# Optimization experiments

Measured on AMD Instinct MI355X. Metric: run time of the kernel, lower is better.

## Reference

```python
import jax, jax.numpy as jnp
import numpy as np

B, T, D, H = 2, 1024, 1024, 16
K = D            # key_dim = hidden * expand_k (1.0)
V = 2 * D        # value_dim = hidden * expand_v (2.0)
DK, DV = K // H, V // H
I = 2816         # SwiGLU intermediate
CONV = 4
EPS = 1e-6


def rmsnorm(x, w, eps=EPS):
    return x * jax.lax.rsqrt(jnp.mean(x * x, -1, keepdims=True) + eps) * w


def l2norm(x, eps=EPS):
    return x * jax.lax.rsqrt(jnp.sum(x * x, -1, keepdims=True) + eps)


def short_conv(x, w):
    # depthwise causal conv1d (kernel CONV, no bias) + silu; x [B,T,C], w [C,CONV]
    kern = w.T[:, None, :]  # [CONV, 1, C]
    y = jax.lax.conv_general_dilated(
        x, kern, (1,), [(CONV - 1, 0)],
        dimension_numbers=('NWC', 'WIO', 'NWC'),
        feature_group_count=x.shape[-1])
    return jax.nn.silu(y)


def setup_inputs() -> dict:
    key = jax.random.key(0)
    ks = jax.random.split(key, 20)
    p = lambda i, shape, s=0.02: jax.random.normal(ks[i], shape, jnp.float32) * s
    return dict(
        x=jax.random.normal(ks[0], (B, T, D), jnp.float32),
        norm1_w=jnp.ones((D,), jnp.float32),
        wq=p(1, (D, K)), wk=p(2, (D, K)), wv=p(3, (D, V)),
        conv_q=p(4, (K, CONV), 0.3), conv_k=p(5, (K, CONV), 0.3), conv_v=p(6, (V, CONV), 0.3),
        wb=p(7, (D, H)), wa=p(8, (D, H)),
        A_log=jnp.log(jax.random.uniform(ks[9], (H,), jnp.float32, 1.0, 16.0)),
        dt_bias=jnp.log(jnp.expm1(jax.random.uniform(ks[10], (H,), jnp.float32, 0.001, 0.1))),
        wg=p(11, (D, V)),
        o_norm_w=jnp.ones((DV,), jnp.float32),
        wo=p(12, (V, D)),
        norm2_w=jnp.ones((D,), jnp.float32),
        w1=p(13, (D, I)), w2=p(14, (I, D)), w3=p(15, (D, I)),
    )


def reference(x, norm1_w, wq, wk, wv, conv_q, conv_k, conv_v, wb, wa,
              A_log, dt_bias, wg, o_norm_w, wo, norm2_w, w1, w2, w3):
    h = rmsnorm(x, norm1_w)
    # projections + short causal conv (silu)
    q = short_conv(h @ wq, conv_q).reshape(B, T, H, DK)
    k = short_conv(h @ wk, conv_k).reshape(B, T, H, DK)
    v = short_conv(h @ wv, conv_v).reshape(B, T, H, DV)
    q = l2norm(q) * (DK ** -0.5)
    k = l2norm(k)
    beta = jax.nn.sigmoid(h @ wb)                              # [B,T,H]
    # mamba-style decay gate: g = -exp(A_log) * softplus(a + dt_bias)
    g = -jnp.exp(A_log) * jax.nn.softplus(h @ wa + dt_bias)   # [B,T,H]

    # gated delta rule: S_t = exp(g_t)*S_{t-1}; u_t = beta_t*(v_t - k_t^T S_t);
    # S_t += k_t u_t^T; o_t = q_t^T S_t
    def step(S, inp):
        qt, kt, vt, gt, bt = inp                               # [B,H,*]
        S = S * jnp.exp(gt)[..., None, None]
        u = (vt - jnp.einsum('bhk,bhkv->bhv', kt, S)) * bt[..., None]
        S = S + kt[..., None] * u[:, :, None, :]
        ot = jnp.einsum('bhk,bhkv->bhv', qt, S)
        return S, ot

    S0 = jnp.zeros((B, H, DK, DV), x.dtype)
    seq = (q.transpose(1, 0, 2, 3), k.transpose(1, 0, 2, 3),
           v.transpose(1, 0, 2, 3), g.transpose(1, 0, 2), beta.transpose(1, 0, 2))
    _, o = jax.lax.scan(step, S0, seq)
    o = o.transpose(1, 0, 2, 3)                                # [B,T,H,DV]

    # output gate: per-head RMSNorm * swish(gate), then out-projection
    gate = (h @ wg).reshape(B, T, H, DV)
    o = rmsnorm(o, o_norm_w) * gate * jax.nn.sigmoid(gate)
    x = x + o.reshape(B, T, V) @ wo

    # SwiGLU MLP with residual
    h2 = rmsnorm(x, norm2_w)
    return x + (jax.nn.silu(h2 @ w1) * (h2 @ w3)) @ w2
```

## Files before the change

kernel.cpp:

```cpp
#include <hip/hip_runtime.h>
#include <stdint.h>

typedef unsigned short u16;
typedef float f32x4 __attribute__((ext_vector_type(4)));
typedef __bf16 bf16x8 __attribute__((ext_vector_type(8)));
typedef unsigned short u16x8 __attribute__((ext_vector_type(8)));

#define N1P 6400

__device__ __forceinline__ u16 f2bf(float f) {
    union { float f; uint32_t u; } v; v.f = f;
    uint32_t u = v.u;
    return (u16)((u + 0x7FFFu + ((u >> 16) & 1u)) >> 16);
}
__device__ __forceinline__ float bf2f(u16 h) {
    union { uint32_t u; float f; } v; v.u = ((uint32_t)h) << 16; return v.f;
}
__device__ __forceinline__ float sigm(float x) { return 1.f / (1.f + __expf(-x)); }

__device__ __forceinline__ void async16(const u16* g, u16* l) {
    __builtin_amdgcn_global_load_lds((const __attribute__((address_space(1))) void*)g,
                                     (__attribute__((address_space(3))) void*)l, 16, 0, 0);
}

__device__ __forceinline__ int swz64(int row, int col) {
    return row * 128 + ((((col >> 3) ^ (row & 7)) << 3) + (col & 7)) * 2;
}
__device__ __forceinline__ bf16x8 frag64(const u16* m, int rowbase, int lane, int kk) {
    const int row = rowbase + (lane & 15);
    const int unit = (lane >> 4) + (kk << 2);
    return *(const bf16x8*)((const char*)m + row * 128 + ((unit ^ (row & 7)) << 4));
}

struct TJob { const float* src; u16* dst; int rows, cols, rowOff, rowStride, nOut, blkBase, gx, mode; };
struct TJobs { TJob j[10]; };

__global__ __launch_bounds__(256) void k_transpose_all(TJobs jobs, int njobs) {
    __shared__ float tile[32][33];
    const int bid = blockIdx.x;
    int ji = 0;
#pragma unroll
    for (int i = 1; i < 10; ++i)
        if (i < njobs && bid >= jobs.j[i].blkBase) ji = i;
    const TJob J = jobs.j[ji];
    const int bx = bid - J.blkBase;
    const int n0 = (bx % J.gx) * 32, k0 = (bx / J.gx) * 32;
    const int tx = threadIdx.x, ty = threadIdx.y;
#pragma unroll
    for (int j = 0; j < 32; j += 8) {
        int r = k0 + ty + j, c = n0 + tx;
        tile[ty + j][tx] = (r < J.rows && c < J.cols) ? J.src[(size_t)r * J.cols + c] : 0.f;
    }
    __syncthreads();
#pragma unroll
    for (int j = 0; j < 32; j += 8) {
        int n = n0 + ty + j, k = k0 + tx;
        if (n < J.nOut) {
            int drow = (J.mode == 0) ? (J.rowOff + n * J.rowStride)
                                     : (J.rowOff + ((n >> 4) << 5) + (n & 15));
            J.dst[(size_t)drow * J.rows + k] = f2bf(tile[tx][ty + j]);
        }
    }
}

__global__ __launch_bounds__(256) void k_rmsnorm(const float* __restrict__ x, const float* __restrict__ w,
                                                 u16* __restrict__ out) {
    const int row = blockIdx.x, tid = threadIdx.x, lane = tid & 63, wave = tid >> 6;
    const float4 v = ((const float4*)(x + (size_t)row * 1024))[tid];
    float ss = v.x * v.x + v.y * v.y + v.z * v.z + v.w * v.w;
#pragma unroll
    for (int o = 1; o < 64; o <<= 1) ss += __shfl_xor(ss, o);
    __shared__ float sred[4];
    if (lane == 0) sred[wave] = ss;
    __syncthreads();
    const float tot = sred[0] + sred[1] + sred[2] + sred[3];
    const float rn = rsqrtf(tot * (1.f / 1024.f) + 1e-6f);
    const float4 wv = ((const float4*)w)[tid];
    uint2 pk;
    pk.x = (uint32_t)f2bf(v.x * rn * wv.x) | ((uint32_t)f2bf(v.y * rn * wv.y) << 16);
    pk.y = (uint32_t)f2bf(v.z * rn * wv.z) | ((uint32_t)f2bf(v.w * rn * wv.w) << 16);
    *(uint2*)&out[(size_t)row * 1024 + tid * 4] = pk;
}

template <int EPI>
__global__ __launch_bounds__(512, 2) void k_gemm256(const u16* __restrict__ A, const u16* __restrict__ Bt,
                                                    u16* __restrict__ Cout, int N, int Kd) {
    __shared__ __align__(16) u16 L[65536];
    const int q8 = (int)gridDim.x >> 3;
    const int bid = blockIdx.x;
    const int wg = (bid & 7) * q8 + (bid >> 3);
    const int bm = wg & 7, bn = wg >> 3;
    const int tid = threadIdx.x, lane = tid & 63, wave = tid >> 6;
    const int wm = wave >> 2, wn = wave & 3;

    const int scol = ((tid & 7) ^ ((tid >> 3) & 7)) * 8;
    const u16* gA = A + (size_t)(bm * 256 + (tid >> 3)) * Kd + scol;
    const u16* gB = Bt + (size_t)(bn * 256 + (tid >> 3)) * Kd + scol;
    u16* dstT = L + tid * 8;

    const int NT = Kd >> 6;
    const int NI = NT >> 1;

    auto issue = [&](const u16* g, int mtx, int kt, int h) {
        u16* d = dstT + (kt & 1) * 32768 + mtx * 16384 + h * 8192;
        const u16* s = g + (size_t)(h * 128) * Kd + kt * 64;
        async16(s, d);
        async16(s + (size_t)64 * Kd, d + 4096);
    };

    issue(gB, 1, 0, 0); issue(gB, 1, 0, 1);
    issue(gA, 0, 0, 0); issue(gA, 0, 0, 1);
    issue(gB, 1, 1, 0); issue(gB, 1, 1, 1);
    asm volatile("s_waitcnt vmcnt(4)" ::: "memory");
    __builtin_amdgcn_s_barrier();

    f32x4 acc[8][4] = {};
    bf16x8 bq[4][2];

    for (int i = 0; i < NI; ++i) {
        const int kt0 = 2 * i;
#pragma unroll
        for (int p = 0; p < 8; ++p) {
            const int half = p >> 2;
            const int q = p & 3;
            const u16* Ab = L + half * 32768;
            const u16* Bb = L + half * 32768 + 16384;
            if (q == 0) {
#pragma unroll
                for (int ni = 0; ni < 4; ++ni)
#pragma unroll
                    for (int kk = 0; kk < 2; ++kk)
                        bq[ni][kk] = frag64(Bb, wn * 64 + ni * 16, lane, kk);
            }
            bf16x8 af[2][2];
#pragma unroll
            for (int j = 0; j < 2; ++j)
#pragma unroll
                for (int kk = 0; kk < 2; ++kk)
                    af[j][kk] = frag64(Ab, wm * 128 + (2 * q + j) * 16, lane, kk);
            if (p == 0) { if (kt0 + 1 < NT) issue(gA, 0, kt0 + 1, 0); }
            if (p == 1) { if (kt0 + 1 < NT) issue(gA, 0, kt0 + 1, 1);
                          if (kt0 + 2 < NT) issue(gB, 1, kt0 + 2, 0); }
            if (p == 2) { if (kt0 + 2 < NT) issue(gB, 1, kt0 + 2, 1); }
            if (p == 4) { if (kt0 + 2 < NT) issue(gA, 0, kt0 + 2, 0); }
            if (p == 5) { if (kt0 + 2 < NT) issue(gA, 0, kt0 + 2, 1);
                          if (kt0 + 3 < NT) issue(gB, 1, kt0 + 3, 0); }
            if (p == 6) { if (kt0 + 3 < NT) issue(gB, 1, kt0 + 3, 1); }
            if (p == 3) { if (i + 1 < NI) { asm volatile("s_waitcnt vmcnt(4)" ::: "memory"); }
                          else            { asm volatile("s_waitcnt vmcnt(0)" ::: "memory"); } }
            if (p == 7) { if (i + 1 < NI) { asm volatile("s_waitcnt vmcnt(4)" ::: "memory"); } }
            __builtin_amdgcn_s_barrier();
            __builtin_amdgcn_s_setprio(1);
#pragma unroll
            for (int j = 0; j < 2; ++j)
#pragma unroll
                for (int ni = 0; ni < 4; ++ni)
#pragma unroll
                    for (int kk = 0; kk < 2; ++kk)
                        acc[2 * q + j][ni] = __builtin_amdgcn_mfma_f32_16x16x32_bf16(
                            af[j][kk], bq[ni][kk], acc[2 * q + j][ni], 0, 0, 0);
            __builtin_amdgcn_s_setprio(0);
            __builtin_amdgcn_s_barrier();
        }
    }

    const int rsub = (lane >> 4) * 4, csub = lane & 15;
    if constexpr (EPI == 2) {
        u16* ct = L;
#pragma unroll
        for (int r = 0; r < 2; ++r) {
            if (wm == r) {
#pragma unroll
                for (int mi = 0; mi < 8; ++mi)
#pragma unroll
                    for (int ni = 0; ni < 4; ++ni)
#pragma unroll
                        for (int rr = 0; rr < 4; ++rr)
                            ct[(mi * 16 + rsub + rr) * 264 + wn * 64 + ni * 16 + csub] =
                                f2bf(acc[mi][ni][rr]);
            }
            __syncthreads();
#pragma unroll
            for (int k = 0; k < 8; ++k) {
                const int f = (tid + k * 512) * 8;
                const int r2 = f >> 8, c = f & 255;
                *(u16x8*)&Cout[(size_t)(bm * 256 + r * 128 + r2) * N + bn * 256 + c] =
                    *(const u16x8*)&ct[r2 * 264 + c];
            }
            __syncthreads();
        }
    } else {
        u16* ct = L;
#pragma unroll
        for (int mi = 0; mi < 8; ++mi)
#pragma unroll
            for (int g = 0; g < 2; ++g)
#pragma unroll
                for (int rr = 0; rr < 4; ++rr) {
                    const float u1 = acc[mi][2 * g][rr];
                    const float u3 = acc[mi][2 * g + 1][rr];
                    ct[(wm * 128 + mi * 16 + rsub + rr) * 132 + wn * 32 + g * 16 + csub] =
                        f2bf(u1 * sigm(u1) * u3);
                }
        __syncthreads();
#pragma unroll
        for (int k = 0; k < 8; ++k) {
            const int f = (tid + k * 512) * 8;
            const int r2 = f >> 7, c = f & 127;
            *(u16x8*)&Cout[(size_t)(bm * 256 + r2) * N + bn * 128 + c] =
                *(const u16x8*)&ct[r2 * 132 + c];
        }
    }
}

template <int TILE, int EPI>
__global__ __launch_bounds__(512) void k_gemm(const u16* __restrict__ A, const u16* __restrict__ Bt,
                                              void* __restrict__ Cout, const float* __restrict__ Res,
                                              int N, int Kd) {
    __shared__ __align__(16) char smem[TILE * 512];
    u16* Asb = (u16*)smem;
    u16* Bsb = (u16*)(smem + TILE * 256);
    constexpr int MB = 2048 / TILE;
    const int q = (int)gridDim.x >> 3;
    const int bid = blockIdx.x;
    const int wg = (bid & 7) * q + (bid >> 3);
    const int bm = wg & (MB - 1), bn = wg / MB;
    const int tid = threadIdx.x, lane = tid & 63, wave = tid >> 6;
    const int wm = wave >> 2, wn = wave & 3;
    constexpr int RS = TILE / 2, CS = TILE / 4;
    constexpr int FRM = RS / 16, FRN = CS / 16;
    constexpr int IS = TILE / 64;

    const int srow = wave * 8 + (lane >> 3);
    const int scol = ((lane & 7) ^ (lane >> 3)) * 8;
    const u16* gA = A + (size_t)(bm * TILE + srow) * Kd + scol;
    const u16* gB = Bt + (size_t)(bn * TILE + srow) * Kd + scol;

    f32x4 acc[FRM][FRN] = {};
    const int NT = Kd >> 6;

#pragma unroll
    for (int j = 0; j < IS; ++j) {
        async16(gA + (size_t)j * 64 * Kd, Asb + j * 4096 + wave * 512);
        async16(gB + (size_t)j * 64 * Kd, Bsb + j * 4096 + wave * 512);
    }
    asm volatile("s_waitcnt vmcnt(0)" ::: "memory");
    __syncthreads();

    int buf = 0;
    for (int t = 0; t < NT; ++t) {
        if (t + 1 < NT) {
            const int k0 = (t + 1) << 6;
            const int bo = (buf ^ 1) * TILE * 64;
#pragma unroll
            for (int j = 0; j < IS; ++j) {
                async16(gA + (size_t)j * 64 * Kd + k0, Asb + bo + j * 4096 + wave * 512);
                async16(gB + (size_t)j * 64 * Kd + k0, Bsb + bo + j * 4096 + wave * 512);
            }
        }
        const u16* Ab = Asb + buf * TILE * 64;
        const u16* Bb = Bsb + buf * TILE * 64;
#pragma unroll
        for (int kk = 0; kk < 2; ++kk) {
            bf16x8 af[FRM], bfr[FRN];
#pragma unroll
            for (int mi = 0; mi < FRM; ++mi) af[mi] = frag64(Ab, wm * RS + mi * 16, lane, kk);
#pragma unroll
            for (int ni = 0; ni < FRN; ++ni) bfr[ni] = frag64(Bb, wn * CS + ni * 16, lane, kk);
#pragma unroll
            for (int mi = 0; mi < FRM; ++mi)
#pragma unroll
                for (int ni = 0; ni < FRN; ++ni)
                    acc[mi][ni] = __builtin_amdgcn_mfma_f32_16x16x32_bf16(af[mi], bfr[ni], acc[mi][ni], 0, 0, 0);
        }
        asm volatile("s_waitcnt vmcnt(0)" ::: "memory");
        __syncthreads();
        buf ^= 1;
    }

    const int rsub = (lane >> 4) * 4;
    const int csub = lane & 15;
    float* ctile = (float*)smem;
#pragma unroll
    for (int mi = 0; mi < FRM; ++mi)
#pragma unroll
        for (int ni = 0; ni < FRN; ++ni)
#pragma unroll
            for (int r = 0; r < 4; ++r)
                ctile[(wm * 32 + mi * 16 + rsub + r) * 68 + wn * 16 + ni * 16 + csub] = acc[mi][ni][r];
    __syncthreads();
#pragma unroll
    for (int k = 0; k < 2; ++k) {
        const int f = (tid + k * 512) * 4;
        const int r = f >> 6, c = f & 63;
        float4 v = *(const float4*)&ctile[r * 68 + c];
        const float4 rv = *(const float4*)&Res[(size_t)(bm * 64 + r) * N + bn * 64 + c];
        v.x += rv.x; v.y += rv.y; v.z += rv.z; v.w += rv.w;
        *(float4*)&((float*)Cout)[(size_t)(bm * 64 + r) * N + bn * 64 + c] = v;
    }
}

__global__ __launch_bounds__(256) void k_conv(const u16* __restrict__ P, const float* __restrict__ cwq,
                                              const float* __restrict__ cwk, const float* __restrict__ cwv,
                                              const float* __restrict__ A_log, const float* __restrict__ dtb,
                                              u16* __restrict__ Qb, u16* __restrict__ Kb,
                                              u16* __restrict__ Vb, float* __restrict__ Gl,
                                              float* __restrict__ Bbuf) {
    const int bid = blockIdx.x;
    const int row = (bid & 7) * 256 + (bid >> 3);
    const int t = row & 1023;
    const int tid = threadIdx.x;
    const long prow = (long)row * N1P;
#pragma unroll
    for (int p = 0; p < 2; ++p) {
        const int g = p * 256 + tid;
        const int c = g * 8;
        u16x8 taps[4];
#pragma unroll
        for (int j = 0; j < 4; ++j) {
            const int tt = t - 3 + j;
            if (tt >= 0) taps[j] = *(const u16x8*)&P[prow + (long)(j - 3) * N1P + c];
            else         taps[j] = u16x8{};
        }
        const float* cw = (c < 1024) ? (cwq + c * 4)
                          : (c < 2048) ? (cwk + (c - 1024) * 4)
                                       : (cwv + (c - 2048) * 4);
        float y[8];
#pragma unroll
        for (int e = 0; e < 8; ++e) {
            const float4 w = ((const float4*)cw)[e];
            float v = bf2f(taps[0][e]) * w.x + bf2f(taps[1][e]) * w.y +
                      bf2f(taps[2][e]) * w.z + bf2f(taps[3][e]) * w.w;
            y[e] = v * sigm(v);
        }
        if (c < 2048) {
            float ss = 0.f;
#pragma unroll
            for (int e = 0; e < 8; ++e) ss += y[e] * y[e];
            ss += __shfl_xor(ss, 1); ss += __shfl_xor(ss, 2); ss += __shfl_xor(ss, 4);
            const float rn = rsqrtf(ss + 1e-6f);
            const float sc = (c < 1024) ? rn * 0.125f : rn;
            u16x8 o;
#pragma unroll
            for (int e = 0; e < 8; ++e) o[e] = f2bf(y[e] * sc);
            if (c < 1024) *(u16x8*)&Qb[(size_t)row * 1024 + c] = o;
            else          *(u16x8*)&Kb[(size_t)row * 1024 + (c - 1024)] = o;
        } else {
            u16x8 o;
#pragma unroll
            for (int e = 0; e < 8; ++e) o[e] = f2bf(y[e]);
            *(u16x8*)&Vb[(size_t)row * 2048 + (c - 2048)] = o;
        }
    }
    if (tid < 32) {
        const int h = tid & 15;
        const float val = bf2f(P[prow + 4096 + tid]);
        if (tid < 16) {
            Bbuf[(size_t)row * 16 + h] = sigm(val);
        } else {
            const float a = val + dtb[h];
            const float sp = (a > 15.f) ? a : log1pf(__expf(a));
            Gl[(size_t)row * 16 + h] = -__expf(A_log[h]) * sp;
        }
    }
}

__global__ __launch_bounds__(256) void k_scan1(
    const u16* __restrict__ Qb, const u16* __restrict__ Kb, const u16* __restrict__ Vb,
    const float* __restrict__ Gl, const float* __restrict__ Bb,
    u16* __restrict__ CHW, u16* __restrict__ CHM, u16* __restrict__ CHQc,
    u16* __restrict__ CHKcT, u16* __restrict__ CHU0T, float* __restrict__ CHcC) {
    __shared__ __align__(16) char sm[66048];
    u16* Ql   = (u16*)(sm);
    u16* Kl   = (u16*)(sm + 8192);
    u16* VTb  = (u16*)(sm + 16384);
    u16* KT1b = (u16*)(sm + 32768);
    u16* Mim  = (u16*)(sm + 40960);
    u16* MTim = (u16*)(sm + 49152);
    u16* Tb   = (u16*)(sm + 57344);
    float* Tl    = (float*)sm;
    float* gcs   = (float*)(sm + 65536);
    float* betal = (float*)(sm + 65792);

    const int blk = blockIdx.x;
    const int bb = blk >> 8, h = (blk >> 4) & 15, ch = blk & 15;
    const int bhc = blk;
    const int tid = threadIdx.x, lane = tid & 63, wave = tid >> 6;
    const long rowbase = (long)bb * 1024 + ch * 64;

    if (tid < 64) {
        gcs[tid] = Gl[(rowbase + tid) * 16 + h];
        betal[tid] = Bb[(rowbase + tid) * 16 + h];
    }
    for (int u = tid; u < 512; u += 256) {
        int r = u >> 3, c8 = u & 7;
        uint4 kv = *(const uint4*)&Kb[(rowbase + r) * 1024 + h * 64 + c8 * 8];
        uint4 qv = *(const uint4*)&Qb[(rowbase + r) * 1024 + h * 64 + c8 * 8];
        int b = r * 128 + ((c8 ^ (r & 7)) << 4);
        *(uint4*)((char*)Kl + b) = kv;
        *(uint4*)((char*)Ql + b) = qv;
    }
    __syncthreads();
    if (wave == 0) {
        float g = gcs[lane];
#pragma unroll
        for (int off = 1; off < 64; off <<= 1) {
            float n = __shfl_up(g, off, 64);
            if (lane >= off) g += n;
        }
        gcs[lane] = g;
    }
    for (int u = tid; u < 1024; u += 256) {
        int r = u >> 4, c8 = u & 15;
        u16x8 vv = *(const u16x8*)&Vb[(rowbase + r) * 2048 + h * 128 + c8 * 8];
        float bsc = betal[r];
#pragma unroll
        for (int j = 0; j < 8; ++j) {
            int dv = c8 * 8 + j;
            *(u16*)((char*)VTb + swz64(dv, r)) = f2bf(bf2f(vv[j]) * bsc);
        }
    }
    f32x4 aQK[4] = {}, aKK[4] = {};
#pragma unroll
    for (int nt = 0; nt < 4; ++nt)
#pragma unroll
        for (int kk = 0; kk < 2; ++kk) {
            bf16x8 bq = frag64(Kl, nt * 16, lane, kk);
            aQK[nt] = __builtin_amdgcn_mfma_f32_16x16x32_bf16(frag64(Ql, wave * 16, lane, kk), bq, aQK[nt], 0, 0, 0);
            aKK[nt] = __builtin_amdgcn_mfma_f32_16x16x32_bf16(frag64(Kl, wave * 16, lane, kk), bq, aKK[nt], 0, 0, 0);
        }
    __syncthreads();

    const float gcsC = gcs[63];
    float am[4][4];
#pragma unroll
    for (int nt = 0; nt < 4; ++nt)
#pragma unroll
        for (int reg = 0; reg < 4; ++reg) {
            int t = wave * 16 + ((lane >> 4) << 2) + reg;
            int i = nt * 16 + (lane & 15);
            float dec = __expf(gcs[t] - gcs[i]);
            float mv = (i <= t) ? dec * aQK[nt][reg] : 0.f;
            *(u16*)((char*)CHM + (size_t)bhc * 8192 + swz64(t, i)) = f2bf(mv);
            float a = (i < t) ? betal[t] * dec * aKK[nt][reg] : 0.f;
            am[nt][reg] = -a;
            u16 amb = f2bf(-a);
            *(u16*)((char*)Mim + swz64(t, i)) = amb;
            *(u16*)((char*)MTim + swz64(i, t)) = amb;
        }
    for (int e = tid; e < 4096; e += 256) {
        int r = e >> 6, c = e & 63;
        int ib = swz64(r, c);
        float qv = bf2f(*(const u16*)((const char*)Ql + ib)) * __expf(gcs[r]);
        *(u16*)((char*)CHQc + (size_t)bhc * 8192 + ib) = f2bf(qv);
        float kv = bf2f(*(const u16*)((const char*)Kl + ib));
        int ob = swz64(c, r);
        *(u16*)((char*)KT1b + ob) = f2bf(kv * betal[r] * __expf(gcs[r]));
        *(u16*)((char*)CHKcT + (size_t)bhc * 8192 + ob) = f2bf(kv * __expf(gcsC - gcs[r]));
    }
    if (tid == 0) CHcC[bhc] = __expf(gcsC);
    __syncthreads();

#pragma unroll
    for (int nt = 0; nt < 4; ++nt)
#pragma unroll
        for (int reg = 0; reg < 4; ++reg) {
            int t = wave * 16 + ((lane >> 4) << 2) + reg;
            int i = nt * 16 + (lane & 15);
            float tv = (t == i) ? 1.f : am[nt][reg];
            Tl[t * 64 + i] = tv;
            *(u16*)((char*)Tb + swz64(t, i)) = f2bf(tv);
        }
    __syncthreads();

    const int hi = wave * 16 + 15;
#pragma unroll
    for (int j = 1; j <= 5; ++j) {
        f32x4 aM[4] = {};
#pragma unroll
        for (int nt = 0; nt < 4; ++nt) {
            if (nt * 16 > hi - (1 << j)) continue;
#pragma unroll
            for (int kk = 0; kk < 2; ++kk) {
                if (kk * 32 > hi) break;
                aM[nt] = __builtin_amdgcn_mfma_f32_16x16x32_bf16(
                    frag64(Mim, wave * 16, lane, kk), frag64(MTim, nt * 16, lane, kk), aM[nt], 0, 0, 0);
            }
        }
        __syncthreads();
#pragma unroll
        for (int nt = 0; nt < 4; ++nt)
#pragma unroll
            for (int reg = 0; reg < 4; ++reg) {
                int t = wave * 16 + ((lane >> 4) << 2) + reg;
                int i = nt * 16 + (lane & 15);
                float mv = (t - i >= (1 << j)) ? aM[nt][reg] : 0.f;
                u16 mb = f2bf(mv);
                *(u16*)((char*)Mim + swz64(t, i)) = mb;
                *(u16*)((char*)MTim + swz64(i, t)) = mb;
            }
        __syncthreads();
        f32x4 aT[4];
#pragma unroll
        for (int nt = 0; nt < 4; ++nt)
#pragma unroll
            for (int reg = 0; reg < 4; ++reg) {
                int t = wave * 16 + ((lane >> 4) << 2) + reg;
                int i = nt * 16 + (lane & 15);
                aT[nt][reg] = Tl[t * 64 + i];
            }
#pragma unroll
        for (int nt = 0; nt < 4; ++nt) {
            if (nt * 16 > hi - (1 << j)) continue;
#pragma unroll
            for (int kk = 0; kk < 2; ++kk) {
                if (kk * 32 > hi) break;
                aT[nt] = __builtin_amdgcn_mfma_f32_16x16x32_bf16(
                    frag64(Tb, wave * 16, lane, kk), frag64(MTim, nt * 16, lane, kk), aT[nt], 0, 0, 0);
            }
        }
#pragma unroll
        for (int nt = 0; nt < 4; ++nt)
#pragma unroll
            for (int reg = 0; reg < 4; ++reg) {
                int t = wave * 16 + ((lane >> 4) << 2) + reg;
                int i = nt * 16 + (lane & 15);
                Tl[t * 64 + i] = aT[nt][reg];
                *(u16*)((char*)Tb + swz64(t, i)) = f2bf(aT[nt][reg]);
            }
    }
    __syncthreads();

    {
        f32x4 aW[4] = {};
#pragma unroll
        for (int nt = 0; nt < 4; ++nt)
#pragma unroll
            for (int kk = 0; kk < 2; ++kk) {
                if (kk * 32 > hi) break;
                aW[nt] = __builtin_amdgcn_mfma_f32_16x16x32_bf16(
                    frag64(Tb, wave * 16, lane, kk), frag64(KT1b, nt * 16, lane, kk), aW[nt], 0, 0, 0);
            }
#pragma unroll
        for (int nt = 0; nt < 4; ++nt)
#pragma unroll
            for (int reg = 0; reg < 4; ++reg) {
                int r = wave * 16 + ((lane >> 4) << 2) + reg;
                int c = nt * 16 + (lane & 15);
                *(u16*)((char*)CHW + (size_t)bhc * 8192 + swz64(r, c)) = f2bf(aW[nt][reg]);
            }
    }
#pragma unroll
    for (int rt = 0; rt < 2; ++rt) {
        f32x4 aU[4] = {};
        int rb = (wave * 2 + rt) * 16;
#pragma unroll
        for (int nt = 0; nt < 4; ++nt)
#pragma unroll
            for (int kk = 0; kk < 2; ++kk) {
                if (kk * 32 > nt * 16 + 15) continue;
                aU[nt] = __builtin_amdgcn_mfma_f32_16x16x32_bf16(
                    frag64(VTb, rb, lane, kk), frag64(Tb, nt * 16, lane, kk), aU[nt], 0, 0, 0);
            }
#pragma unroll
        for (int nt = 0; nt < 4; ++nt)
#pragma unroll
            for (int reg = 0; reg < 4; ++reg) {
                int dv = rb + ((lane >> 4) << 2) + reg;
                int c = nt * 16 + (lane & 15);
                *(u16*)((char*)CHU0T + (size_t)bhc * 16384 + swz64(dv, c)) = f2bf(aU[nt][reg]);
            }
    }
}

__global__ __launch_bounds__(256) void k_scan2(
    const u16* __restrict__ CHW, const u16* __restrict__ CHM, const u16* __restrict__ CHQc,
    const u16* __restrict__ CHKcT, const u16* __restrict__ CHU0T, const float* __restrict__ CHcC,
    float* __restrict__ O) {
    __shared__ __align__(16) u16 stg[2][5 * 4096];
    __shared__ __align__(16) u16 STb[4096], uTl[4096];
    __shared__ float ST[64 * 66];
    const int blk = blockIdx.x;
    const int bb = blk >> 5, h = (blk >> 1) & 15, dvh = blk & 1;
    const int bh = bb * 16 + h;
    const int tid = threadIdx.x, lane = tid & 63, wave = tid >> 6;

    for (int e = tid; e < 64 * 66; e += 256) ST[e] = 0.f;
    for (int e = tid; e < 4096; e += 256) STb[e] = 0;

    auto stage = [&](int buf, int ch) {
        const size_t base = (size_t)(bh * 16 + ch);
        const u16* srcs[5] = { CHW + base * 4096, CHM + base * 4096, CHQc + base * 4096,
                               CHKcT + base * 4096, CHU0T + base * 8192 + dvh * 4096 };
#pragma unroll
        for (int s = 0; s < 5; ++s)
#pragma unroll
            for (int r = 0; r < 2; ++r) {
                int ub = r * 256 + wave * 64;
                async16(srcs[s] + (size_t)(ub + lane) * 8, &stg[buf][s * 4096 + ub * 8]);
            }
    };
    stage(0, 0);
    for (int ch = 0; ch < 16; ++ch) {
        const int cur = ch & 1;
        asm volatile("s_waitcnt vmcnt(0)" ::: "memory");
        __syncthreads();
        if (ch < 15) stage(cur ^ 1, ch + 1);
        const u16* sW = &stg[cur][0];
        const u16* sM = &stg[cur][4096];
        const u16* sQc = &stg[cur][8192];
        const u16* sKcT = &stg[cur][12288];
        const u16* sU0 = &stg[cur][16384];
        {
            f32x4 acc[4] = {};
#pragma unroll
            for (int nt = 0; nt < 4; ++nt)
#pragma unroll
                for (int kk = 0; kk < 2; ++kk)
                    acc[nt] = __builtin_amdgcn_mfma_f32_16x16x32_bf16(
                        frag64(STb, wave * 16, lane, kk), frag64(sW, nt * 16, lane, kk), acc[nt], 0, 0, 0);
#pragma unroll
            for (int nt = 0; nt < 4; ++nt)
#pragma unroll
                for (int reg = 0; reg < 4; ++reg) {
                    int dv = wave * 16 + ((lane >> 4) << 2) + reg;
                    int c = nt * 16 + (lane & 15);
                    int b = swz64(dv, c);
                    float u0 = bf2f(*(const u16*)((const char*)sU0 + b));
                    *(u16*)((char*)uTl + b) = f2bf(u0 - acc[nt][reg]);
                }
        }
        __syncthreads();
        f32x4 accO[4] = {}, accS[4] = {};
#pragma unroll
        for (int nt = 0; nt < 4; ++nt)
#pragma unroll
            for (int kk = 0; kk < 2; ++kk) {
                accO[nt] = __builtin_amdgcn_mfma_f32_16x16x32_bf16(
                    frag64(sM, wave * 16, lane, kk), frag64(uTl, nt * 16, lane, kk), accO[nt], 0, 0, 0);
                accO[nt] = __builtin_amdgcn_mfma_f32_16x16x32_bf16(
                    frag64(sQc, wave * 16, lane, kk), frag64(STb, nt * 16, lane, kk), accO[nt], 0, 0, 0);
                accS[nt] = __builtin_amdgcn_mfma_f32_16x16x32_bf16(
                    frag64(uTl, wave * 16, lane, kk), frag64(sKcT, nt * 16, lane, kk), accS[nt], 0, 0, 0);
            }
        __syncthreads();
        const float cC = CHcC[bh * 16 + ch];
#pragma unroll
        for (int nt = 0; nt < 4; ++nt)
#pragma unroll
            for (int reg = 0; reg < 4; ++reg) {
                int rr = wave * 16 + ((lane >> 4) << 2) + reg;
                int cc = nt * 16 + (lane & 15);
                O[((size_t)(bb * 1024 + ch * 64 + rr)) * 2048 + h * 128 + dvh * 64 + cc] = accO[nt][reg];
                float ns = cC * ST[rr * 66 + cc] + accS[nt][reg];
                ST[rr * 66 + cc] = ns;
                *(u16*)((char*)STb + swz64(rr, cc)) = f2bf(ns);
            }
    }
}

__global__ __launch_bounds__(256) void k_gate(const float* __restrict__ O, const u16* __restrict__ P,
                                              const float* __restrict__ onw, u16* __restrict__ OG) {
    const int row = blockIdx.x;
    const int tid = threadIdx.x, lane = tid & 63, wave = tid >> 6;
#pragma unroll
    for (int p = 0; p < 4; ++p) {
        const int h = p * 4 + wave;
        const int dv = lane * 2;
        const float2 o2 = *(const float2*)&O[(size_t)row * 2048 + h * 128 + dv];
        float ss = o2.x * o2.x + o2.y * o2.y;
#pragma unroll
        for (int o = 1; o < 64; o <<= 1) ss += __shfl_xor(ss, o);
        const float rn = rsqrtf(ss * (1.f / 128.f) + 1e-6f);
        const float g0 = bf2f(P[(size_t)row * N1P + 4128 + h * 128 + dv]);
        const float g1 = bf2f(P[(size_t)row * N1P + 4128 + h * 128 + dv + 1]);
        const float r0 = o2.x * rn * onw[dv] * g0 * sigm(g0);
        const float r1 = o2.y * rn * onw[dv + 1] * g1 * sigm(g1);
        const uint32_t pk = (uint32_t)f2bf(r0) | ((uint32_t)f2bf(r1) << 16);
        *(uint32_t*)&OG[(size_t)row * 2048 + h * 128 + dv] = pk;
    }
}

extern "C" void kernel_launch(void* const* d_in, const int* in_sizes, int n_in,
                              void* d_out, int out_size, void* d_ws, size_t ws_size,
                              hipStream_t stream) {
    const float* x   = (const float*)d_in[0];
    const float* n1w = (const float*)d_in[1];
    const float* wq  = (const float*)d_in[2];
    const float* wk  = (const float*)d_in[3];
    const float* wv  = (const float*)d_in[4];
    const float* cq  = (const float*)d_in[5];
    const float* ck  = (const float*)d_in[6];
    const float* cv  = (const float*)d_in[7];
    const float* wb  = (const float*)d_in[8];
    const float* wa  = (const float*)d_in[9];
    const float* Alg = (const float*)d_in[10];
    const float* dtb = (const float*)d_in[11];
    const float* wg  = (const float*)d_in[12];
    const float* onw = (const float*)d_in[13];
    const float* wo  = (const float*)d_in[14];
    const float* n2w = (const float*)d_in[15];
    const float* w1  = (const float*)d_in[16];
    const float* w2  = (const float*)d_in[17];
    const float* w3  = (const float*)d_in[18];

    if (ws_size < 111413248ULL) return;

    char* ws = (char*)d_ws;
    u16*   WcatT = (u16*)(ws + 0);
    u16*   WoT   = (u16*)(ws + 13107200);
    u16*   W13T  = (u16*)(ws + 17301504);
    u16*   W2T   = (u16*)(ws + 28835840);
    u16*   hA    = (u16*)(ws + 34603008);
    u16*   P     = (u16*)(ws + 38797312);
    u16*   Qb    = (u16*)(ws + 65011712);
    u16*   Kb    = (u16*)(ws + 69206016);
    u16*   Vb    = (u16*)(ws + 73400320);
    float* Gl    = (float*)(ws + 81788928);
    float* Bbf   = (float*)(ws + 81920000);
    float* O     = (float*)(ws + 82051072);
    u16*   CHKcT = (u16*)(ws + 98828288);
    u16*   CHU0T = (u16*)(ws + 103022592);
    float* CHcC  = (float*)(ws + 111411200);
    u16*   CHW   = WcatT;
    u16*   CHM   = (u16*)(ws + 4194304);
    u16*   CHQc  = (u16*)(ws + 8388608);
    u16*   Mm  = Qb;
    u16*   OG  = Vb;
    float* X2  = O;
    u16*   h2A = hA;

    TJobs tj;
    tj.j[0] = { wq, WcatT, 1024, 1024,    0, 1, 1024,     0, 32, 0 };
    tj.j[1] = { wk, WcatT, 1024, 1024, 1024, 1, 1024,  1024, 32, 0 };
    tj.j[2] = { wv, WcatT, 1024, 2048, 2048, 1, 2048,  2048, 64, 0 };
    tj.j[3] = { wb, WcatT, 1024,   16, 4096, 1,   16,  4096,  1, 0 };
    tj.j[4] = { wa, WcatT, 1024,   16, 4112, 1,   16,  4128,  1, 0 };
    tj.j[5] = { wg, WcatT, 1024, 2048, 4128, 1, 2272,  4160, 71, 0 };
    tj.j[6] = { wo, WoT,   2048, 1024,    0, 1, 1024,  6432, 32, 0 };
    tj.j[7] = { w1, W13T,  1024, 2816,    0, 1, 2816,  8480, 88, 1 };
    tj.j[8] = { w3, W13T,  1024, 2816,   16, 1, 2816, 11296, 88, 1 };
    tj.j[9] = { w2, W2T,   2816, 1024,    0, 1, 1024, 14112, 32, 0 };
    k_transpose_all<<<16928, dim3(32, 8), 0, stream>>>(tj, 10);

    k_rmsnorm<<<2048, 256, 0, stream>>>(x, n1w, hA);
    k_gemm256<2><<<200, 512, 0, stream>>>(hA, WcatT, P, N1P, 1024);

    k_conv<<<2048, 256, 0, stream>>>(P, cq, ck, cv, Alg, dtb, Qb, Kb, Vb, Gl, Bbf);

    k_scan1<<<512, 256, 0, stream>>>(Qb, Kb, Vb, Gl, Bbf, CHW, CHM, CHQc, CHKcT, CHU0T, CHcC);
    k_scan2<<<64, 256, 0, stream>>>(CHW, CHM, CHQc, CHKcT, CHU0T, CHcC, O);

    k_gate<<<2048, 256, 0, stream>>>(O, P, onw, OG);
    k_gemm<64, 1><<<512, 512, 0, stream>>>(OG, WoT, X2, x, 1024, 2048);

    k_rmsnorm<<<2048, 256, 0, stream>>>(X2, n2w, h2A);
    k_gemm256<3><<<176, 512, 0, stream>>>(h2A, W13T, Mm, 2816, 1024);
    k_gemm<64, 1><<<512, 512, 0, stream>>>(Mm, W2T, (float*)d_out, X2, 1024, 2816);
}
```

Measured before the change: 242.3 us.

## Split chunk scan into state-only pass and parallel output pass fused with gate

The sequential chunk scan now only propagates the state and writes per-chunk corrected values u and the chunk-start states to workspace. A new 512-block kernel computes each chunk's outputs in parallel and fuses the per-head RMSNorm and swish gating that the separate gate kernel used to do, which removes the fp32 O round trip. The two residual GEMMs also switch from 64x64 tiles to 128x64 tiles with 256 blocks. The cost is extra workspace traffic for u and S0, and fewer blocks for the output GEMMs.

After: 259.0 us (median of 2 runs). +6.9%, slower.

```diff
diff --git a/kernel.cpp b/kernel.cpp
--- a/kernel.cpp
+++ b/kernel.cpp
@@ -213,37 +213,30 @@
     }
 }
 
-template <int TILE, int EPI>
-__global__ __launch_bounds__(512) void k_gemm(const u16* __restrict__ A, const u16* __restrict__ Bt,
-                                              void* __restrict__ Cout, const float* __restrict__ Res,
-                                              int N, int Kd) {
-    __shared__ __align__(16) char smem[TILE * 512];
+__global__ __launch_bounds__(512) void k_gemm_skinny(const u16* __restrict__ A, const u16* __restrict__ Bt,
+                                                     float* __restrict__ Cout, const float* __restrict__ Res,
+                                                     int N, int Kd) {
+    __shared__ __align__(16) char smem[49152];
     u16* Asb = (u16*)smem;
-    u16* Bsb = (u16*)(smem + TILE * 256);
-    constexpr int MB = 2048 / TILE;
+    u16* Bsb = (u16*)(smem + 32768);
     const int q = (int)gridDim.x >> 3;
     const int bid = blockIdx.x;
     const int wg = (bid & 7) * q + (bid >> 3);
-    const int bm = wg & (MB - 1), bn = wg / MB;
+    const int bm = wg & 15, bn = wg >> 4;
     const int tid = threadIdx.x, lane = tid & 63, wave = tid >> 6;
-    const int wm = wave >> 2, wn = wave & 3;
-    constexpr int RS = TILE / 2, CS = TILE / 4;
-    constexpr int FRM = RS / 16, FRN = CS / 16;
-    constexpr int IS = TILE / 64;
-
-    const int srow = wave * 8 + (lane >> 3);
-    const int scol = ((lane & 7) ^ (lane >> 3)) * 8;
-    const u16* gA = A + (size_t)(bm * TILE + srow) * Kd + scol;
-    const u16* gB = Bt + (size_t)(bn * TILE + srow) * Kd + scol;
-
-    f32x4 acc[FRM][FRN] = {};
+    const int wm = wave >> 1, wn = wave & 1;
+
+    const int srow = tid >> 3;
+    const int scol = ((tid & 7) ^ ((tid >> 3) & 7)) * 8;
+    const u16* gA = A + (size_t)(bm * 128 + srow) * Kd + scol;
+    const u16* gB = Bt + (size_t)(bn * 64 + srow) * Kd + scol;
+
+    f32x4 acc[2][2] = {};
     const int NT = Kd >> 6;
 
-#pragma unroll
-    for (int j = 0; j < IS; ++j) {
-        async16(gA + (size_t)j * 64 * Kd, Asb + j * 4096 + wave * 512);
-        async16(gB + (size_t)j * 64 * Kd, Bsb + j * 4096 + wave * 512);
-    }
+    async16(gA, Asb + wave * 512);
+    async16(gA + (size_t)64 * Kd, Asb + 4096 + wave * 512);
+    async16(gB, Bsb + wave * 512);
     asm volatile("s_waitcnt vmcnt(0)" ::: "memory");
     __syncthreads();
 
@@ -251,26 +244,24 @@
     for (int t = 0; t < NT; ++t) {
         if (t + 1 < NT) {
             const int k0 = (t + 1) << 6;
-            const int bo = (buf ^ 1) * TILE * 64;
-#pragma unroll
-            for (int j = 0; j < IS; ++j) {
-                async16(gA + (size_t)j * 64 * Kd + k0, Asb + bo + j * 4096 + wave * 512);
-                async16(gB + (size_t)j * 64 * Kd + k0, Bsb + bo + j * 4096 + wave * 512);
-            }
-        }
-        const u16* Ab = Asb + buf * TILE * 64;
-        const u16* Bb = Bsb + buf * TILE * 64;
+            const int ba = (buf ^ 1) * 8192, bb2 = (buf ^ 1) * 4096;
+            async16(gA + k0, Asb + ba + wave * 512);
+            async16(gA + (size_t)64 * Kd + k0, Asb + ba + 4096 + wave * 512);
+            async16(gB + k0, Bsb + bb2 + wave * 512);
+        }
+        const u16* Ab = Asb + buf * 8192;
+        const u16* Bb = Bsb + buf * 4096;
 #pragma unroll
         for (int kk = 0; kk < 2; ++kk) {
-            bf16x8 af[FRM], bfr[FRN];
-#pragma unroll
-            for (int mi = 0; mi < FRM; ++mi) af[mi] = frag64(Ab, wm * RS + mi * 16, lane, kk);
-#pragma unroll
-            for (int ni = 0; ni < FRN; ++ni) bfr[ni] = frag64(Bb, wn * CS + ni * 16, lane, kk);
-#pragma unroll
-            for (int mi = 0; mi < FRM; ++mi)
-#pragma unroll
-                for (int ni = 0; ni < FRN; ++ni)
+            bf16x8 af[2], bfr[2];
+#pragma unroll
+            for (int mi = 0; mi < 2; ++mi) af[mi] = frag64(Ab, wm * 32 + mi * 16, lane, kk);
+#pragma unroll
+            for (int ni = 0; ni < 2; ++ni) bfr[ni] = frag64(Bb, wn * 32 + ni * 16, lane, kk);
+#pragma unroll
+            for (int mi = 0; mi < 2; ++mi)
+#pragma unroll
+                for (int ni = 0; ni < 2; ++ni)
                     acc[mi][ni] = __builtin_amdgcn_mfma_f32_16x16x32_bf16(af[mi], bfr[ni], acc[mi][ni], 0, 0, 0);
         }
         asm volatile("s_waitcnt vmcnt(0)" ::: "memory");
@@ -282,21 +273,21 @@
     const int csub = lane & 15;
     float* ctile = (float*)smem;
 #pragma unroll
-    for (int mi = 0; mi < FRM; ++mi)
-#pragma unroll
-        for (int ni = 0; ni < FRN; ++ni)
+    for (int mi = 0; mi < 2; ++mi)
+#pragma unroll
+        for (int ni = 0; ni < 2; ++ni)
 #pragma unroll
             for (int r = 0; r < 4; ++r)
-                ctile[(wm * 32 + mi * 16 + rsub + r) * 68 + wn * 16 + ni * 16 + csub] = acc[mi][ni][r];
-    __syncthreads();
-#pragma unroll
-    for (int k = 0; k < 2; ++k) {
+                ctile[(wm * 32 + mi * 16 + rsub + r) * 68 + wn * 32 + ni * 16 + csub] = acc[mi][ni][r];
+    __syncthreads();
+#pragma unroll
+    for (int k = 0; k < 4; ++k) {
         const int f = (tid + k * 512) * 4;
         const int r = f >> 6, c = f & 63;
         float4 v = *(const float4*)&ctile[r * 68 + c];
-        const float4 rv = *(const float4*)&Res[(size_t)(bm * 64 + r) * N + bn * 64 + c];
+        const float4 rv = *(const float4*)&Res[(size_t)(bm * 128 + r) * N + bn * 64 + c];
         v.x += rv.x; v.y += rv.y; v.z += rv.z; v.w += rv.w;
-        *(float4*)&((float*)Cout)[(size_t)(bm * 64 + r) * N + bn * 64 + c] = v;
+        *(float4*)&Cout[(size_t)(bm * 128 + r) * N + bn * 64 + c] = v;
     }
 }
 
@@ -574,10 +565,9 @@
 }
 
 __global__ __launch_bounds__(256) void k_scan2(
-    const u16* __restrict__ CHW, const u16* __restrict__ CHM, const u16* __restrict__ CHQc,
-    const u16* __restrict__ CHKcT, const u16* __restrict__ CHU0T, const float* __restrict__ CHcC,
-    float* __restrict__ O) {
-    __shared__ __align__(16) u16 stg[2][5 * 4096];
+    const u16* __restrict__ CHW, const u16* __restrict__ CHKcT, const u16* __restrict__ CHU0T,
+    const float* __restrict__ CHcC, u16* __restrict__ CHu, u16* __restrict__ CHS0) {
+    __shared__ __align__(16) u16 stg[2][3 * 4096];
     __shared__ __align__(16) u16 STb[4096], uTl[4096];
     __shared__ float ST[64 * 66];
     const int blk = blockIdx.x;
@@ -590,10 +580,10 @@
 
     auto stage = [&](int buf, int ch) {
         const size_t base = (size_t)(bh * 16 + ch);
-        const u16* srcs[5] = { CHW + base * 4096, CHM + base * 4096, CHQc + base * 4096,
-                               CHKcT + base * 4096, CHU0T + base * 8192 + dvh * 4096 };
-#pragma unroll
-        for (int s = 0; s < 5; ++s)
+        const u16* srcs[3] = { CHW + base * 4096, CHKcT + base * 4096,
+                               CHU0T + base * 8192 + dvh * 4096 };
+#pragma unroll
+        for (int s = 0; s < 3; ++s)
 #pragma unroll
             for (int r = 0; r < 2; ++r) {
                 int ub = r * 256 + wave * 64;
@@ -607,10 +597,8 @@
         __syncthreads();
         if (ch < 15) stage(cur ^ 1, ch + 1);
         const u16* sW = &stg[cur][0];
-        const u16* sM = &stg[cur][4096];
-        const u16* sQc = &stg[cur][8192];
-        const u16* sKcT = &stg[cur][12288];
-        const u16* sU0 = &stg[cur][16384];
+        const u16* sKcT = &stg[cur][4096];
+        const u16* sU0 = &stg[cur][8192];
         {
             f32x4 acc[4] = {};
 #pragma unroll
@@ -619,6 +607,7 @@
                 for (int kk = 0; kk < 2; ++kk)
                     acc[nt] = __builtin_amdgcn_mfma_f32_16x16x32_bf16(
                         frag64(STb, wave * 16, lane, kk), frag64(sW, nt * 16, lane, kk), acc[nt], 0, 0, 0);
+            const size_t ubase = ((size_t)(bh * 16 + ch) * 2 + dvh) * 8192;
 #pragma unroll
             for (int nt = 0; nt < 4; ++nt)
 #pragma unroll
@@ -627,57 +616,128 @@
                     int c = nt * 16 + (lane & 15);
                     int b = swz64(dv, c);
                     float u0 = bf2f(*(const u16*)((const char*)sU0 + b));
-                    *(u16*)((char*)uTl + b) = f2bf(u0 - acc[nt][reg]);
+                    u16 uv = f2bf(u0 - acc[nt][reg]);
+                    *(u16*)((char*)uTl + b) = uv;
+                    *(u16*)((char*)CHu + ubase + b) = uv;
                 }
         }
         __syncthreads();
-        f32x4 accO[4] = {}, accS[4] = {};
-#pragma unroll
-        for (int nt = 0; nt < 4; ++nt)
-#pragma unroll
-            for (int kk = 0; kk < 2; ++kk) {
-                accO[nt] = __builtin_amdgcn_mfma_f32_16x16x32_bf16(
-                    frag64(sM, wave * 16, lane, kk), frag64(uTl, nt * 16, lane, kk), accO[nt], 0, 0, 0);
-                accO[nt] = __builtin_amdgcn_mfma_f32_16x16x32_bf16(
-                    frag64(sQc, wave * 16, lane, kk), frag64(STb, nt * 16, lane, kk), accO[nt], 0, 0, 0);
+        f32x4 accS[4] = {};
+#pragma unroll
+        for (int nt = 0; nt < 4; ++nt)
+#pragma unroll
+            for (int kk = 0; kk < 2; ++kk)
                 accS[nt] = __builtin_amdgcn_mfma_f32_16x16x32_bf16(
                     frag64(uTl, wave * 16, lane, kk), frag64(sKcT, nt * 16, lane, kk), accS[nt], 0, 0, 0);
-            }
         __syncthreads();
         const float cC = CHcC[bh * 16 + ch];
+        const size_t sbase = ((size_t)(bh * 16 + ch + 1) * 2 + dvh) * 8192;
 #pragma unroll
         for (int nt = 0; nt < 4; ++nt)
 #pragma unroll
             for (int reg = 0; reg < 4; ++reg) {
                 int rr = wave * 16 + ((lane >> 4) << 2) + reg;
                 int cc = nt * 16 + (lane & 15);
-                O[((size_t)(bb * 1024 + ch * 64 + rr)) * 2048 + h * 128 + dvh * 64 + cc] = accO[nt][reg];
                 float ns = cC * ST[rr * 66 + cc] + accS[nt][reg];
                 ST[rr * 66 + cc] = ns;
-                *(u16*)((char*)STb + swz64(rr, cc)) = f2bf(ns);
-            }
-    }
-}
-
-__global__ __launch_bounds__(256) void k_gate(const float* __restrict__ O, const u16* __restrict__ P,
-                                              const float* __restrict__ onw, u16* __restrict__ OG) {
-    const int row = blockIdx.x;
+                u16 nb = f2bf(ns);
+                *(u16*)((char*)STb + swz64(rr, cc)) = nb;
+                if (ch < 15) *(u16*)((char*)CHS0 + sbase + swz64(rr, cc)) = nb;
+            }
+    }
+}
+
+__global__ __launch_bounds__(256) void k_scan3(
+    const u16* __restrict__ CHM, const u16* __restrict__ CHQc, const u16* __restrict__ CHu,
+    const u16* __restrict__ CHS0, const u16* __restrict__ P, const float* __restrict__ onw,
+    u16* __restrict__ OG) {
+    __shared__ __align__(16) char sm3[65536];
+    u16* sM  = (u16*)sm3;
+    u16* sQc = (u16*)(sm3 + 8192);
+    u16* sU  = (u16*)(sm3 + 16384);
+    u16* sS0 = (u16*)(sm3 + 32768);
+    u16* sPg = (u16*)(sm3 + 49152);
+    const int blk = blockIdx.x;
+    const int bb = blk >> 8, h = (blk >> 4) & 15, ch = blk & 15;
+    const size_t bhc = blk;
     const int tid = threadIdx.x, lane = tid & 63, wave = tid >> 6;
-#pragma unroll
-    for (int p = 0; p < 4; ++p) {
-        const int h = p * 4 + wave;
-        const int dv = lane * 2;
-        const float2 o2 = *(const float2*)&O[(size_t)row * 2048 + h * 128 + dv];
-        float ss = o2.x * o2.x + o2.y * o2.y;
-#pragma unroll
-        for (int o = 1; o < 64; o <<= 1) ss += __shfl_xor(ss, o);
-        const float rn = rsqrtf(ss * (1.f / 128.f) + 1e-6f);
-        const float g0 = bf2f(P[(size_t)row * N1P + 4128 + h * 128 + dv]);
-        const float g1 = bf2f(P[(size_t)row * N1P + 4128 + h * 128 + dv + 1]);
-        const float r0 = o2.x * rn * onw[dv] * g0 * sigm(g0);
-        const float r1 = o2.y * rn * onw[dv + 1] * g1 * sigm(g1);
-        const uint32_t pk = (uint32_t)f2bf(r0) | ((uint32_t)f2bf(r1) << 16);
-        *(uint32_t*)&OG[(size_t)row * 2048 + h * 128 + dv] = pk;
+    const bool hasS0 = (ch != 0);
+
+#pragma unroll
+    for (int r = 0; r < 2; ++r) {
+        const int ub = r * 256 + wave * 64;
+        async16(CHM + bhc * 4096 + (size_t)(ub + lane) * 8, sM + ub * 8);
+        async16(CHQc + bhc * 4096 + (size_t)(ub + lane) * 8, sQc + ub * 8);
+#pragma unroll
+        for (int d = 0; d < 2; ++d) {
+            async16(CHu + (bhc * 2 + d) * 4096 + (size_t)(ub + lane) * 8, sU + d * 4096 + ub * 8);
+            if (hasS0)
+                async16(CHS0 + (bhc * 2 + d) * 4096 + (size_t)(ub + lane) * 8, sS0 + d * 4096 + ub * 8);
+        }
+    }
+    const long prow0 = ((long)bb * 1024 + ch * 64) * N1P + 4128 + h * 128;
+#pragma unroll
+    for (int k = 0; k < 4; ++k) {
+        const int i = tid + k * 256;
+        const int row = i >> 4, seg = i & 15;
+        async16(P + prow0 + (long)row * N1P + seg * 8, sPg + i * 8);
+    }
+    asm volatile("s_waitcnt vmcnt(0)" ::: "memory");
+    __syncthreads();
+
+    f32x4 accO[2][4] = {};
+#pragma unroll
+    for (int d = 0; d < 2; ++d)
+#pragma unroll
+        for (int nt = 0; nt < 4; ++nt)
+#pragma unroll
+            for (int kk = 0; kk < 2; ++kk) {
+                accO[d][nt] = __builtin_amdgcn_mfma_f32_16x16x32_bf16(
+                    frag64(sM, wave * 16, lane, kk), frag64(sU + d * 4096, nt * 16, lane, kk),
+                    accO[d][nt], 0, 0, 0);
+                if (hasS0)
+                    accO[d][nt] = __builtin_amdgcn_mfma_f32_16x16x32_bf16(
+                        frag64(sQc, wave * 16, lane, kk), frag64(sS0 + d * 4096, nt * 16, lane, kk),
+                        accO[d][nt], 0, 0, 0);
+            }
+
+    const int rsub = (lane >> 4) * 4, csub = lane & 15;
+    float rn[4];
+#pragma unroll
+    for (int reg = 0; reg < 4; ++reg) {
+        float ss = 0.f;
+#pragma unroll
+        for (int d = 0; d < 2; ++d)
+#pragma unroll
+            for (int nt = 0; nt < 4; ++nt) {
+                const float v = accO[d][nt][reg];
+                ss += v * v;
+            }
+        ss += __shfl_xor(ss, 1); ss += __shfl_xor(ss, 2);
+        ss += __shfl_xor(ss, 4); ss += __shfl_xor(ss, 8);
+        rn[reg] = rsqrtf(ss * (1.f / 128.f) + 1e-6f);
+    }
+    __syncthreads();
+    u16* ct = (u16*)sm3;
+#pragma unroll
+    for (int d = 0; d < 2; ++d)
+#pragma unroll
+        for (int nt = 0; nt < 4; ++nt)
+#pragma unroll
+            for (int reg = 0; reg < 4; ++reg) {
+                const int rr = wave * 16 + rsub + reg;
+                const int dv = d * 64 + nt * 16 + csub;
+                const float g = bf2f(sPg[rr * 128 + dv]);
+                const float val = accO[d][nt][reg] * rn[reg] * onw[dv] * g * sigm(g);
+                ct[rr * 136 + dv] = f2bf(val);
+            }
+    __syncthreads();
+#pragma unroll
+    for (int k = 0; k < 4; ++k) {
+        const int f = (tid + k * 256) * 8;
+        const int r2 = f >> 7, c = f & 127;
+        *(u16x8*)&OG[(size_t)(bb * 1024 + ch * 64 + r2) * 2048 + h * 128 + c] =
+            *(const u16x8*)&ct[r2 * 136 + c];
     }
 }
 
@@ -704,7 +764,7 @@
     const float* w2  = (const float*)d_in[17];
     const float* w3  = (const float*)d_in[18];
 
-    if (ws_size < 111413248ULL) return;
+    if (ws_size < 128190464ULL) return;
 
     char* ws = (char*)d_ws;
     u16*   WcatT = (u16*)(ws + 0);
@@ -718,16 +778,17 @@
     u16*   Vb    = (u16*)(ws + 73400320);
     float* Gl    = (float*)(ws + 81788928);
     float* Bbf   = (float*)(ws + 81920000);
-    float* O     = (float*)(ws + 82051072);
+    float* X2    = (float*)(ws + 82051072);
     u16*   CHKcT = (u16*)(ws + 98828288);
     u16*   CHU0T = (u16*)(ws + 103022592);
     float* CHcC  = (float*)(ws + 111411200);
+    u16*   CHu   = (u16*)(ws + 111413248);
+    u16*   CHS0  = (u16*)(ws + 119801856);
     u16*   CHW   = WcatT;
     u16*   CHM   = (u16*)(ws + 4194304);
     u16*   CHQc  = (u16*)(ws + 8388608);
     u16*   Mm  = Qb;
     u16*   OG  = Vb;
-    float* X2  = O;
     u16*   h2A = hA;
 
     TJobs tj;
@@ -749,12 +810,12 @@
     k_conv<<<2048, 256, 0, stream>>>(P, cq, ck, cv, Alg, dtb, Qb, Kb, Vb, Gl, Bbf);
 
     k_scan1<<<512, 256, 0, stream>>>(Qb, Kb, Vb, Gl, Bbf, CHW, CHM, CHQc, CHKcT, CHU0T, CHcC);
-    k_scan2<<<64, 256, 0, stream>>>(CHW, CHM, CHQc, CHKcT, CHU0T, CHcC, O);
-
-    k_gate<<<2048, 256, 0, stream>>>(O, P, onw, OG);
-    k_gemm<64, 1><<<512, 512, 0, stream>>>(OG, WoT, X2, x, 1024, 2048);
+    k_scan2<<<64, 256, 0, stream>>>(CHW, CHKcT, CHU0T, CHcC, CHu, CHS0);
+    k_scan3<<<512, 256, 0, stream>>>(CHM, CHQc, CHu, CHS0, P, onw, OG);
+
+    k_gemm_skinny<<<256, 512, 0, stream>>>(OG, WoT, X2, x, 1024, 2048);
 
     k_rmsnorm<<<2048, 256, 0, stream>>>(X2, n2w, h2A);
     k_gemm256<3><<<176, 512, 0, stream>>>(h2A, W13T, Mm, 2816, 1024);
-    k_gemm<64, 1><<<512, 512, 0, stream>>>(Mm, W2T, (float*)d_out, X2, 1024, 2816);
-}
+    k_gemm_skinny<<<256, 512, 0, stream>>>(Mm, W2T, (float*)d_out, X2, 1024, 2816);
+}
```
